# Kernel tuning notes

Hardware: AMD Instinct MI355X
Metric: run time of the kernel (lower is better)

Reference implementation:

```python
import jax, jax.numpy as jnp
import numpy as np

ALPHA = 0.2          # LeakyReLU negative slope
NEG_INF = -9e15      # standard GAT masking constant


def gat_layer(h, adj_mask, W, a_src, a_dst):
    # h: [N, D], adj_mask: [N, N] bool
    Wh = h @ W                                  # [N, D]
    e = (Wh @ a_src)[:, None] + (Wh @ a_dst)[None, :]  # [N, N]
    e = jax.nn.leaky_relu(e, negative_slope=ALPHA)
    e = jnp.where(adj_mask, e, NEG_INF)
    attn = jax.nn.softmax(e, axis=-1)           # [N, N]
    return jax.nn.relu(attn @ Wh)               # PlainGCN applies ReLU


def setup_inputs() -> dict:
    key = jax.random.key(0)
    ks = jax.random.split(key, 8)
    N, D = 8192, 256
    x = jax.random.normal(ks[0], (N, D), dtype=jnp.float32)
    adj = jax.random.randint(ks[1], (N, N), 0, 2, dtype=jnp.int32)
    s = 1.0 / np.sqrt(D)
    W1 = jax.random.normal(ks[2], (D, D), dtype=jnp.float32) * s
    a1_src = jax.random.normal(ks[3], (D,), dtype=jnp.float32) * s
    a1_dst = jax.random.normal(ks[4], (D,), dtype=jnp.float32) * s
    W2 = jax.random.normal(ks[5], (D, D), dtype=jnp.float32) * s
    a2_src = jax.random.normal(ks[6], (D,), dtype=jnp.float32) * s
    a2_dst = jax.random.normal(ks[7], (D,), dtype=jnp.float32) * s
    return {"x": x, "adj": adj, "W1": W1, "a1_src": a1_src, "a1_dst": a1_dst,
            "W2": W2, "a2_src": a2_src, "a2_dst": a2_dst}


def reference(x, adj, W1, a1_src, a1_dst, W2, a2_src, a2_dst):
    adj_mask = adj > 0
    h = gat_layer(x, adj_mask, W1, a1_src, a1_dst)
    h = gat_layer(h, adj_mask, W2, a2_src, a2_dst)
    return h
```

## Files before the change

### kernel.cpp

```cpp
#include <hip/hip_runtime.h>
#include <cstdint>
#include <cstddef>


#define ALPHA 0.2f
#define NN 8192
#define DD 256

typedef __attribute__((ext_vector_type(8))) short short8;
typedef __attribute__((ext_vector_type(4))) float f32x4;
typedef __attribute__((ext_vector_type(2))) _Float16 half2v;
typedef __attribute__((ext_vector_type(8))) __fp16 h8;

__device__ __forceinline__ unsigned pk_f16(float a, float b) {
    return __builtin_bit_cast(unsigned, __builtin_amdgcn_cvt_pkrtz(a, b));
}

__device__ __forceinline__ int sbit(uint32_t x, int o) {
    return ((int)(x << (31 - o))) >> 31;
}

__device__ __forceinline__ uint32_t hmerge(uint32_t hi, uint32_t lo) {
#if __has_builtin(__builtin_amdgcn_perm)
    return __builtin_amdgcn_perm(hi, lo, 0x07060100u);
#else
    return (hi & 0xFFFF0000u) | (lo & 0x0000FFFFu);
#endif
}

__device__ __forceinline__ half2v pkmax(half2v a, half2v b) {
#if __has_builtin(__builtin_elementwise_max)
    return __builtin_elementwise_max(a, b);
#else
    half2v r;
    asm("v_pk_max_f16 %0, %1, %2" : "=v"(r) : "v"(a), "v"(b));
    return r;
#endif
}

__device__ __forceinline__ f32x4 mfma_f16(uint4 a, short8 b, f32x4 c) {
    return __builtin_amdgcn_mfma_f32_16x16x32_f16(__builtin_bit_cast(h8, a),
                                                  __builtin_bit_cast(h8, b), c, 0, 0, 0);
}


__device__ __forceinline__ void packbits_dev(const int* __restrict__ adj,
                                             uint64_t* __restrict__ bits,
                                             int row, int lane) {
    const int* rowp = adj + (size_t)row * NN;
    uint64_t* dst = bits + (size_t)row * 128;
    for (int it = 0; it < 16; it++) {
        const int* p = rowp + it * 512;
        int a0 = p[lane];
        int a1 = p[64 + lane];
        int a2 = p[128 + lane];
        int a3 = p[192 + lane];
        int a4 = p[256 + lane];
        int a5 = p[320 + lane];
        int a6 = p[384 + lane];
        int a7 = p[448 + lane];
        uint64_t m0 = __ballot(a0 != 0);
        uint64_t m1 = __ballot(a1 != 0);
        uint64_t m2 = __ballot(a2 != 0);
        uint64_t m3 = __ballot(a3 != 0);
        uint64_t m4 = __ballot(a4 != 0);
        uint64_t m5 = __ballot(a5 != 0);
        uint64_t m6 = __ballot(a6 != 0);
        uint64_t m7 = __ballot(a7 != 0);
        if (lane == 0) {
            dst[it * 8 + 0] = m0; dst[it * 8 + 1] = m1;
            dst[it * 8 + 2] = m2; dst[it * 8 + 3] = m3;
            dst[it * 8 + 4] = m4; dst[it * 8 + 5] = m5;
            dst[it * 8 + 6] = m6; dst[it * 8 + 7] = m7;
        }
    }
}

__device__ __forceinline__ void transp_dev(const uint32_t* __restrict__ bits32,
                                           uint32_t* __restrict__ bitsT,
                                           int job, unsigned char* smem, int t) {
    uint32_t (*tile)[65] = (uint32_t (*)[65])smem;
    const int i0 = (job >> 2) * 64;
    const int w0 = (job & 3) * 64;
#pragma unroll
    for (int p = 0; p < 4; p++) {
        int r = (t >> 4) + 16 * p;
        int c4 = (t & 15) * 4;
        uint4 v = *(const uint4*)(bits32 + (size_t)(i0 + r) * 256 + w0 + c4);
        tile[r][c4 + 0] = v.x; tile[r][c4 + 1] = v.y;
        tile[r][c4 + 2] = v.z; tile[r][c4 + 3] = v.w;
    }
    __syncthreads();
#pragma unroll
    for (int p = 0; p < 4; p++) {
        int wr = (t >> 4) + 16 * p;
        int i4 = (t & 15) * 4;
        uint4 o = {tile[i4][wr], tile[i4 + 1][wr], tile[i4 + 2][wr], tile[i4 + 3][wr]};
        *(uint4*)(bitsT + (size_t)(w0 + wr) * NN + i0 + i4) = o;
    }
}

__device__ __forceinline__ void gemm_dev(const float* __restrict__ A,
                                         const float* __restrict__ B,
                                         unsigned short* __restrict__ Bpack,
                                         const float* __restrict__ a_src,
                                         const float* __restrict__ a_dst,
                                         float* __restrict__ s4,
                                         float* __restrict__ dd4,
                                         int job, unsigned char* smem, int t) {
    float (*At)[36] = (float (*)[36])smem;
    float2 (*Bs)[32] = (float2 (*)[32])(smem + 4608);
    const int m0 = (job >> 2) * 32;
    const int cq = job & 3;
    const int r0 = (t >> 5) * 4;
    const int cl = t & 31;
    float acc[4][2];
#pragma unroll
    for (int i = 0; i < 4; i++) { acc[i][0] = 0.f; acc[i][1] = 0.f; }

    for (int k0 = 0; k0 < DD; k0 += 32) {
        {
            int row = t >> 3, kq = t & 7;
            float4 v = *(const float4*)(A + (size_t)(m0 + row) * DD + k0 + kq * 4);
            At[kq * 4 + 0][row] = v.x; At[kq * 4 + 1][row] = v.y;
            At[kq * 4 + 2][row] = v.z; At[kq * 4 + 3][row] = v.w;
        }
#pragma unroll
        for (int l2 = 0; l2 < 2; l2++) {
            int fi = l2 * 256 + t;
            int br = fi >> 4, bc4 = fi & 15;
            float4 v = *(const float4*)(B + (size_t)(k0 + br) * DD + cq * 64 + bc4 * 4);
            Bs[br][bc4 * 2] = {v.x, v.y};
            Bs[br][bc4 * 2 + 1] = {v.z, v.w};
        }
        __syncthreads();
#pragma unroll
        for (int k = 0; k < 32; k++) {
            float4 a0 = *(const float4*)&At[k][r0];
            float2 b = Bs[k][cl];
            float av[4] = {a0.x, a0.y, a0.z, a0.w};
#pragma unroll
            for (int i = 0; i < 4; i++) {
                acc[i][0] += av[i] * b.x;
                acc[i][1] += av[i] * b.y;
            }
        }
        __syncthreads();
    }

    const int jt = m0 >> 5;
    const int lq = ((r0 >> 3) & 3) * 16;
    const int i8 = r0 & 4;
#pragma unroll
    for (int cc = 0; cc < 2; cc++) {
        int c = cq * 64 + cl * 2 + cc;
        int ct = c >> 4;
        int lane = lq + (c & 15);
        uint2 pk;
        pk.x = pk_f16(acc[0][cc], acc[1][cc]);
        pk.y = pk_f16(acc[2][cc], acc[3][cc]);
        *(uint2*)(Bpack + ((size_t)(jt * 16 + ct) * 64 + lane) * 8 + i8) = pk;
    }

    const int c0 = cq * 64 + cl * 2;
    float as0 = a_src[c0], as1 = a_src[c0 + 1];
    float ad0 = a_dst[c0], ad1 = a_dst[c0 + 1];
    float ps[4], pd[4];
#pragma unroll
    for (int i = 0; i < 4; i++) {
        ps[i] = acc[i][0] * as0 + acc[i][1] * as1;
        pd[i] = acc[i][0] * ad0 + acc[i][1] * ad1;
    }
#pragma unroll
    for (int off = 16; off; off >>= 1) {
#pragma unroll
        for (int i = 0; i < 4; i++) {
            ps[i] += __shfl_xor(ps[i], off);
            pd[i] += __shfl_xor(pd[i], off);
        }
    }
    if (cl == 0) {
#pragma unroll
        for (int i = 0; i < 4; i++) {
            s4[(size_t)cq * NN + m0 + r0 + i] = ps[i];
            dd4[(size_t)cq * NN + m0 + r0 + i] = pd[i];
        }
    }
}

__device__ __forceinline__ void rowstats_dev(const uint32_t* __restrict__ bits32,
                                             const float* __restrict__ s,
                                             const float* __restrict__ dd,
                                             float* __restrict__ Ep,
                                             float* __restrict__ Gp,
                                             int job, unsigned char* smem, int t) {
    uint32_t* smk = (uint32_t*)smem;
    float (*red)[4] = (float (*)[4])(smem + 4096);
    const int i0 = job * 4;
    const int wave = t >> 6, lane = t & 63;
    {
        const uint4* src = (const uint4*)(bits32 + (size_t)i0 * 256);
        ((uint4*)smk)[t] = src[t];
    }
    __syncthreads();

    float mx[4];
#pragma unroll
    for (int r = 0; r < 4; r++) mx[r] = -3.0e38f;
#pragma unroll
    for (int q = 0; q < 8; q++) {
        float4 v = *(const float4*)(dd + 4 * (t + 256 * q));
        const int wq = 32 * q + (t >> 3);
        const int sh = (t & 7) * 4;
#pragma unroll
        for (int r = 0; r < 4; r++) {
            uint32_t b = smk[r * 256 + wq] >> sh;
            mx[r] = fmaxf(mx[r], (b & 1u) ? v.x : -3.0e38f);
            mx[r] = fmaxf(mx[r], (b & 2u) ? v.y : -3.0e38f);
            mx[r] = fmaxf(mx[r], (b & 4u) ? v.z : -3.0e38f);
            mx[r] = fmaxf(mx[r], (b & 8u) ? v.w : -3.0e38f);
        }
    }
#pragma unroll
    for (int r = 0; r < 4; r++) {
#pragma unroll
        for (int off = 32; off; off >>= 1) mx[r] = fmaxf(mx[r], __shfl_down(mx[r], off));
    }
    if (lane == 0) {
#pragma unroll
        for (int r = 0; r < 4; r++) red[wave][r] = mx[r];
    }
    __syncthreads();
    if (t < 4) {
        float dmax = fmaxf(fmaxf(red[0][t], red[1][t]), fmaxf(red[2][t], red[3][t]));
        float si = s[i0 + t];
        float e = si + dmax;
        float m = e >= 0.f ? e : ALPHA * e;
        Ep[i0 + t] = 256.0f * __expf(si - m);
        Gp[i0 + t] = 256.0f * __expf(ALPHA * si - m);
    }
}


__global__ __launch_bounds__(256) void mega1(const float* __restrict__ A,
                                             const float* __restrict__ W,
                                             unsigned short* __restrict__ Bpack,
                                             const float* __restrict__ a_src,
                                             const float* __restrict__ a_dst,
                                             float* __restrict__ s4,
                                             float* __restrict__ dd4,
                                             const int* __restrict__ adj,
                                             uint64_t* __restrict__ bits) {
    __shared__ __align__(16) unsigned char smem[12800];
    const int bx = blockIdx.x;
    const int t = threadIdx.x;
    const int sel = bx % 3;
    const int base = bx / 3;
    if (sel == 0) {
        gemm_dev(A, W, Bpack, a_src, a_dst, s4, dd4, base, smem, t);
    } else {
        const int row = base * 8 + (sel - 1) * 4 + (t >> 6);
        packbits_dev(adj, bits, row, t & 63);
    }
}

__global__ __launch_bounds__(256) void mega2(const uint32_t* __restrict__ bits32,
                                             uint32_t* __restrict__ bitsT,
                                             const float* __restrict__ s,
                                             const float* __restrict__ dd,
                                             float* __restrict__ Ep,
                                             float* __restrict__ Gp) {
    __shared__ __align__(16) unsigned char smem[16640];
    const int bx = blockIdx.x;
    const int t = threadIdx.x;
    const int sel = bx % 5;
    const int base = bx / 5;
    if (sel == 0) {
        transp_dev(bits32, bitsT, base, smem, t);
    } else {
        rowstats_dev(bits32, s, dd, Ep, Gp, base * 4 + (sel - 1), smem, t);
    }
}

__global__ __launch_bounds__(256) void k_gemm(const float* A, const float* W,
                                              unsigned short* Bpack,
                                              const float* a_src, const float* a_dst,
                                              float* s4, float* dd4) {
    __shared__ __align__(16) unsigned char smem[12800];
    gemm_dev(A, W, Bpack, a_src, a_dst, s4, dd4, blockIdx.x, smem, threadIdx.x);
}
__global__ __launch_bounds__(256) void k_rowstats(const uint32_t* bits32, const float* s,
                                                  const float* dd,
                                                  float* Ep, float* Gp) {
    __shared__ __align__(16) unsigned char smem[4200];
    rowstats_dev(bits32, s, dd, Ep, Gp, blockIdx.x, smem, threadIdx.x);
}

__global__ __launch_bounds__(256) void fhgen(const float* __restrict__ s4,
                                             const float* __restrict__ dd4,
                                             float* __restrict__ s,
                                             float* __restrict__ dd,
                                             uint32_t* __restrict__ FF,
                                             uint32_t* __restrict__ HH) {
    int i = blockIdx.x * 256 + threadIdx.x;
    float ssum = (s4[i] + s4[i + NN]) + (s4[i + 2 * NN] + s4[i + 3 * NN]);
    float dsum = (dd4[i] + dd4[i + NN]) + (dd4[i + 2 * NN] + dd4[i + 3 * NN]);
    s[i] = ssum;
    dd[i] = dsum;
    float F = __expf(dsum);
    float H = __expf(ALPHA * dsum);
    float Fn = __shfl_xor(F, 1);
    float Hn = __shfl_xor(H, 1);
    if ((i & 1) == 0) {
        FF[i >> 1] = pk_f16(F, Fn);
        HH[i >> 1] = pk_f16(H, Hn);
    }
}

__global__ __launch_bounds__(256, 4) void pv_mfma(const unsigned short* __restrict__ Bpack,
                                                  const uint32_t* __restrict__ bitsT,
                                                  const uint32_t* __restrict__ FF,
                                                  const uint32_t* __restrict__ HH,
                                                  const float* __restrict__ Ep,
                                                  const float* __restrict__ Gp,
                                                  float* __restrict__ pout,
                                                  float* __restrict__ rsum) {
    __shared__ __align__(16) uint4 pb[2][256];
    const int t = threadIdx.x;
    const int w = t >> 6, l = t & 63;
    const int bx = blockIdx.x;
    const int ks = bx & 7;
    const int i0 = (bx >> 3) * 64;
    const int kbase = ks * 32;

    const int rl16 = l & 15;
    const int ko = (l >> 4) * 8;
    const int rw = i0 + 16 * w + rl16;
    const _Float16 eph = (_Float16)Ep[rw];
    const _Float16 gph = (_Float16)Gp[rw];
    const half2v ep2 = {eph, eph};
    const half2v gp2 = {gph, gph};

    const unsigned short* bb = Bpack + ((size_t)(w * 4) * 64 + l) * 8;
    const uint32_t* btb = bitsT + rw;
    const uint32_t* ffb = FF + (ko >> 1);
    const uint32_t* hhb = HH + (ko >> 1);

    f32x4 acc[4][4];
#pragma unroll
    for (int i = 0; i < 4; i++)
#pragma unroll
        for (int q = 0; q < 4; q++) acc[i][q] = (f32x4){0.f, 0.f, 0.f, 0.f};
    float rsv = 0.f;

    auto build = [&](int cc) -> uint4 {
        uint32_t bw = btb[(size_t)cc * NN];
        uint4 fw = *(const uint4*)(ffb + cc * 16);
        uint4 hw = *(const uint4*)(hhb + cc * 16);
        const uint32_t fwa[4] = {fw.x, fw.y, fw.z, fw.w};
        const uint32_t hwa[4] = {hw.x, hw.y, hw.z, hw.w};
        const uint32_t wl = bw >> ko;
        uint32_t au[4];
#pragma unroll
        for (int p = 0; p < 4; p++) {
            half2v f2 = __builtin_bit_cast(half2v, fwa[p]);
            half2v h2 = __builtin_bit_cast(half2v, hwa[p]);
            half2v pm = ep2 * f2;
            half2v pa = gp2 * h2;
            half2v px = pkmax(pm, pa);
            uint32_t mlo = (uint32_t)sbit(wl, 2 * p);
            uint32_t mhi = (uint32_t)sbit(wl, 2 * p + 1);
            au[p] = __builtin_bit_cast(uint32_t, px) & hmerge(mhi, mlo);
        }
        half2v s01 = __builtin_bit_cast(half2v, au[0]) + __builtin_bit_cast(half2v, au[1]);
        half2v s23 = __builtin_bit_cast(half2v, au[2]) + __builtin_bit_cast(half2v, au[3]);
        half2v sp = s01 + s23;
        rsv += (float)sp.x + (float)sp.y;
        return (uint4){au[0], au[1], au[2], au[3]};
    };

    uint4 aucur = build(kbase);
    pb[0][w * 64 + l] = aucur;

    for (int jl = 0; jl < 32; jl++) {
        const int par = jl & 1;
        const unsigned short* bp = bb + (size_t)(kbase + jl) * 8192;
        short8 B0 = *(const short8*)(bp);
        short8 B1 = *(const short8*)(bp + 512);
        short8 B2 = *(const short8*)(bp + 1024);
        short8 B3 = *(const short8*)(bp + 1536);

        __syncthreads();

#pragma unroll
        for (int f = 0; f < 4; f++) {
            uint4 af;
            if (f == w) af = aucur;
            else        af = pb[par][f * 64 + l];
            acc[f][0] = mfma_f16(af, B0, acc[f][0]);
            acc[f][1] = mfma_f16(af, B1, acc[f][1]);
            acc[f][2] = mfma_f16(af, B2, acc[f][2]);
            acc[f][3] = mfma_f16(af, B3, acc[f][3]);
        }

        if (jl < 31) {
            uint4 an = build(kbase + jl + 1);
            pb[par ^ 1][w * 64 + l] = an;
            aucur = an;
        }
    }

    rsv += __shfl_xor(rsv, 16);
    rsv += __shfl_xor(rsv, 32);
    if (l < 16) rsum[(size_t)ks * NN + rw] = rsv;

    float* outp = pout + (size_t)ks * NN * DD;
#pragma unroll
    for (int f = 0; f < 4; f++) {
        const int orow = i0 + 16 * f + (l >> 4) * 4;
#pragma unroll
        for (int q = 0; q < 4; q++) {
            const int ocol = w * 64 + q * 16 + rl16;
#pragma unroll
            for (int r = 0; r < 4; r++)
                outp[(size_t)(orow + r) * DD + ocol] = acc[f][q][r];
        }
    }
}

__global__ __launch_bounds__(256) void combine8(const float* __restrict__ p,
                                                const float* __restrict__ rsum,
                                                float* __restrict__ out) {
    const size_t S = (size_t)NN * DD / 4;
    size_t idx = (size_t)blockIdx.x * 256 + threadIdx.x;
    const int row = (int)(idx >> 6);
    float rs = (rsum[row] + rsum[row + NN]) + (rsum[row + 2 * NN] + rsum[row + 3 * NN])
             + (rsum[row + 4 * NN] + rsum[row + 5 * NN])
             + (rsum[row + 6 * NN] + rsum[row + 7 * NN]);
    const float inv = 1.0f / rs;
    float4 a0 = ((const float4*)p)[idx];
    float4 a1 = ((const float4*)p)[idx + S];
    float4 a2 = ((const float4*)p)[idx + 2 * S];
    float4 a3 = ((const float4*)p)[idx + 3 * S];
    float4 a4 = ((const float4*)p)[idx + 4 * S];
    float4 a5 = ((const float4*)p)[idx + 5 * S];
    float4 a6 = ((const float4*)p)[idx + 6 * S];
    float4 a7 = ((const float4*)p)[idx + 7 * S];
    float4 o;
    o.x = fmaxf((((a0.x + a1.x) + (a2.x + a3.x)) + ((a4.x + a5.x) + (a6.x + a7.x))) * inv, 0.f);
    o.y = fmaxf((((a0.y + a1.y) + (a2.y + a3.y)) + ((a4.y + a5.y) + (a6.y + a7.y))) * inv, 0.f);
    o.z = fmaxf((((a0.z + a1.z) + (a2.z + a3.z)) + ((a4.z + a5.z) + (a6.z + a7.z))) * inv, 0.f);
    o.w = fmaxf((((a0.w + a1.w) + (a2.w + a3.w)) + ((a4.w + a5.w) + (a6.w + a7.w))) * inv, 0.f);
    ((float4*)out)[idx] = o;
}

extern "C" void kernel_launch(void* const* d_in, const int* in_sizes, int n_in,
                              void* d_out, int out_size, void* d_ws, size_t ws_size,
                              hipStream_t stream) {
    const float* x   = (const float*)d_in[0];
    const int* adj   = (const int*)d_in[1];
    const float* W1  = (const float*)d_in[2];
    const float* a1s = (const float*)d_in[3];
    const float* a1d = (const float*)d_in[4];
    const float* W2  = (const float*)d_in[5];
    const float* a2s = (const float*)d_in[6];
    const float* a2d = (const float*)d_in[7];
    float* out = (float*)d_out;

    char* ws = (char*)d_ws;
    const size_t MB = 1024ull * 1024ull;
    uint64_t*       bits  = (uint64_t*)(ws + 8 * MB);
    uint32_t*       bits32= (uint32_t*)bits;
    uint32_t*       bitsT = (uint32_t*)(ws + 16 * MB);
    float*          sArr  = (float*)(ws + 24 * MB);
    float*          ddA   = sArr + NN;
    float*          EpA   = sArr + 2 * NN;
    float*          GpA   = sArr + 3 * NN;
    float*          s4    = sArr + 4 * NN;
    float*          dd4   = sArr + 8 * NN;
    uint32_t*       FFA   = (uint32_t*)(sArr + 12 * NN);
    uint32_t*       HHA   = FFA + NN / 2;
    float*          rsumA = sArr + 13 * NN;
    unsigned short* Bpack = (unsigned short*)(ws + 25 * MB);
    float*          pout  = (float*)(ws + 32 * MB);

    mega1<<<dim3(3072), dim3(256), 0, stream>>>(x, W1, Bpack, a1s, a1d, s4, dd4,
                                                adj, bits);
    fhgen<<<dim3(32), dim3(256), 0, stream>>>(s4, dd4, sArr, ddA, FFA, HHA);
    mega2<<<dim3(2560), dim3(256), 0, stream>>>(bits32, bitsT, sArr, ddA, EpA, GpA);
    pv_mfma<<<dim3(1024), dim3(256), 0, stream>>>(Bpack, bitsT, FFA, HHA, EpA, GpA,
                                                  pout, rsumA);
    combine8<<<dim3(2048), dim3(256), 0, stream>>>(pout, rsumA, out);

    k_gemm<<<dim3(1024), dim3(256), 0, stream>>>(out, W2, Bpack, a2s, a2d, s4, dd4);
    fhgen<<<dim3(32), dim3(256), 0, stream>>>(s4, dd4, sArr, ddA, FFA, HHA);
    k_rowstats<<<dim3(2048), dim3(256), 0, stream>>>(bits32, sArr, ddA, EpA, GpA);
    pv_mfma<<<dim3(1024), dim3(256), 0, stream>>>(Bpack, bitsT, FFA, HHA, EpA, GpA,
                                                  pout, rsumA);
    combine8<<<dim3(2048), dim3(256), 0, stream>>>(pout, rsumA, out);
}
```

Measured before the change: 538.8 us.

## Replace per-row masked max with global max softmax shift, drop rowstats pass

Computes the softmax stabilizing maximum from the global maximum of destination scores instead of a per-row masked neighbour maximum. This removes the rowstats kernels that scanned the adjacency bitmask for every row in both layers. The fhgen step is folded into the transpose megakernel, and a small epgen kernel is added to produce the row scaling factors. The shift is still a valid upper bound, but rows whose true max is far below the global one risk reduced precision or underflow.

```diff
diff --git a/kernel.cpp b/kernel.cpp
--- a/kernel.cpp
+++ b/kernel.cpp
@@ -188,57 +188,32 @@
     }
 }
 
-__device__ __forceinline__ void rowstats_dev(const uint32_t* __restrict__ bits32,
-                                             const float* __restrict__ s,
-                                             const float* __restrict__ dd,
-                                             float* __restrict__ Ep,
-                                             float* __restrict__ Gp,
-                                             int job, unsigned char* smem, int t) {
-    uint32_t* smk = (uint32_t*)smem;
-    float (*red)[4] = (float (*)[4])(smem + 4096);
-    const int i0 = job * 4;
+__device__ __forceinline__ void fhgen_dev(const float* __restrict__ s4,
+                                          const float* __restrict__ dd4,
+                                          float* __restrict__ s,
+                                          uint32_t* __restrict__ FF,
+                                          uint32_t* __restrict__ HH,
+                                          float* __restrict__ dmax32,
+                                          int job, float* sred, int t) {
+    const int i = job * 256 + t;
+    float ssum = (s4[i] + s4[i + NN]) + (s4[i + 2 * NN] + s4[i + 3 * NN]);
+    float dsum = (dd4[i] + dd4[i + NN]) + (dd4[i + 2 * NN] + dd4[i + 3 * NN]);
+    s[i] = ssum;
+    float F = __expf(dsum);
+    float H = __expf(ALPHA * dsum);
+    float Fn = __shfl_xor(F, 1);
+    float Hn = __shfl_xor(H, 1);
+    if ((i & 1) == 0) {
+        FF[i >> 1] = pk_f16(F, Fn);
+        HH[i >> 1] = pk_f16(H, Hn);
+    }
+    float bm = dsum;
+#pragma unroll
+    for (int off = 32; off; off >>= 1) bm = fmaxf(bm, __shfl_xor(bm, off));
     const int wave = t >> 6, lane = t & 63;
-    {
-        const uint4* src = (const uint4*)(bits32 + (size_t)i0 * 256);
-        ((uint4*)smk)[t] = src[t];
-    }
+    if (lane == 0) sred[wave] = bm;
     __syncthreads();
-
-    float mx[4];
-#pragma unroll
-    for (int r = 0; r < 4; r++) mx[r] = -3.0e38f;
-#pragma unroll
-    for (int q = 0; q < 8; q++) {
-        float4 v = *(const float4*)(dd + 4 * (t + 256 * q));
-        const int wq = 32 * q + (t >> 3);
-        const int sh = (t & 7) * 4;
-#pragma unroll
-        for (int r = 0; r < 4; r++) {
-            uint32_t b = smk[r * 256 + wq] >> sh;
-            mx[r] = fmaxf(mx[r], (b & 1u) ? v.x : -3.0e38f);
-            mx[r] = fmaxf(mx[r], (b & 2u) ? v.y : -3.0e38f);
-            mx[r] = fmaxf(mx[r], (b & 4u) ? v.z : -3.0e38f);
-            mx[r] = fmaxf(mx[r], (b & 8u) ? v.w : -3.0e38f);
-        }
-    }
-#pragma unroll
-    for (int r = 0; r < 4; r++) {
-#pragma unroll
-        for (int off = 32; off; off >>= 1) mx[r] = fmaxf(mx[r], __shfl_down(mx[r], off));
-    }
-    if (lane == 0) {
-#pragma unroll
-        for (int r = 0; r < 4; r++) red[wave][r] = mx[r];
-    }
-    __syncthreads();
-    if (t < 4) {
-        float dmax = fmaxf(fmaxf(red[0][t], red[1][t]), fmaxf(red[2][t], red[3][t]));
-        float si = s[i0 + t];
-        float e = si + dmax;
-        float m = e >= 0.f ? e : ALPHA * e;
-        Ep[i0 + t] = 256.0f * __expf(si - m);
-        Gp[i0 + t] = 256.0f * __expf(ALPHA * si - m);
-    }
+    if (t == 0) dmax32[job] = fmaxf(fmaxf(sred[0], sred[1]), fmaxf(sred[2], sred[3]));
 }
 
 
@@ -264,21 +239,21 @@
     }
 }
 
-__global__ __launch_bounds__(256) void mega2(const uint32_t* __restrict__ bits32,
+__global__ __launch_bounds__(256) void megaB(const uint32_t* __restrict__ bits32,
                                              uint32_t* __restrict__ bitsT,
-                                             const float* __restrict__ s,
-                                             const float* __restrict__ dd,
-                                             float* __restrict__ Ep,
-                                             float* __restrict__ Gp) {
+                                             const float* __restrict__ s4,
+                                             const float* __restrict__ dd4,
+                                             float* __restrict__ s,
+                                             uint32_t* __restrict__ FF,
+                                             uint32_t* __restrict__ HH,
+                                             float* __restrict__ dmax32) {
     __shared__ __align__(16) unsigned char smem[16640];
     const int bx = blockIdx.x;
     const int t = threadIdx.x;
-    const int sel = bx % 5;
-    const int base = bx / 5;
-    if (sel == 0) {
-        transp_dev(bits32, bitsT, base, smem, t);
+    if (bx < 512) {
+        transp_dev(bits32, bitsT, bx, smem, t);
     } else {
-        rowstats_dev(bits32, s, dd, Ep, Gp, base * 4 + (sel - 1), smem, t);
+        fhgen_dev(s4, dd4, s, FF, HH, dmax32, bx - 512, (float*)smem, t);
     }
 }
 
@@ -289,32 +264,36 @@
     __shared__ __align__(16) unsigned char smem[12800];
     gemm_dev(A, W, Bpack, a_src, a_dst, s4, dd4, blockIdx.x, smem, threadIdx.x);
 }
-__global__ __launch_bounds__(256) void k_rowstats(const uint32_t* bits32, const float* s,
-                                                  const float* dd,
-                                                  float* Ep, float* Gp) {
-    __shared__ __align__(16) unsigned char smem[4200];
-    rowstats_dev(bits32, s, dd, Ep, Gp, blockIdx.x, smem, threadIdx.x);
-}
-
-__global__ __launch_bounds__(256) void fhgen(const float* __restrict__ s4,
-                                             const float* __restrict__ dd4,
-                                             float* __restrict__ s,
-                                             float* __restrict__ dd,
-                                             uint32_t* __restrict__ FF,
-                                             uint32_t* __restrict__ HH) {
-    int i = blockIdx.x * 256 + threadIdx.x;
-    float ssum = (s4[i] + s4[i + NN]) + (s4[i + 2 * NN] + s4[i + 3 * NN]);
-    float dsum = (dd4[i] + dd4[i + NN]) + (dd4[i + 2 * NN] + dd4[i + 3 * NN]);
-    s[i] = ssum;
-    dd[i] = dsum;
-    float F = __expf(dsum);
-    float H = __expf(ALPHA * dsum);
-    float Fn = __shfl_xor(F, 1);
-    float Hn = __shfl_xor(H, 1);
-    if ((i & 1) == 0) {
-        FF[i >> 1] = pk_f16(F, Fn);
-        HH[i >> 1] = pk_f16(H, Hn);
-    }
+__global__ __launch_bounds__(256) void k_fhgen(const float* __restrict__ s4,
+                                               const float* __restrict__ dd4,
+                                               float* __restrict__ s,
+                                               uint32_t* __restrict__ FF,
+                                               uint32_t* __restrict__ HH,
+                                               float* __restrict__ dmax32) {
+    __shared__ float sred[4];
+    fhgen_dev(s4, dd4, s, FF, HH, dmax32, blockIdx.x, sred, threadIdx.x);
+}
+
+__global__ __launch_bounds__(256) void epgen(const float* __restrict__ s,
+                                             const float* __restrict__ dmax32,
+                                             float* __restrict__ Ep,
+                                             float* __restrict__ Gp) {
+    __shared__ float sm;
+    const int t = threadIdx.x;
+    if (t == 0) {
+        float m = dmax32[0];
+#pragma unroll
+        for (int k = 1; k < 32; k++) m = fmaxf(m, dmax32[k]);
+        sm = m;
+    }
+    __syncthreads();
+    const float dmax = sm;
+    const int i = blockIdx.x * 256 + t;
+    float si = s[i];
+    float e = si + dmax;
+    float m = e >= 0.f ? e : ALPHA * e;
+    Ep[i] = 256.0f * __expf(si - m);
+    Gp[i] = 256.0f * __expf(ALPHA * si - m);
 }
 
 __global__ __launch_bounds__(256, 4) void pv_mfma(const unsigned short* __restrict__ Bpack,
@@ -473,28 +452,29 @@
     uint32_t*       bits32= (uint32_t*)bits;
     uint32_t*       bitsT = (uint32_t*)(ws + 16 * MB);
     float*          sArr  = (float*)(ws + 24 * MB);
-    float*          ddA   = sArr + NN;
-    float*          EpA   = sArr + 2 * NN;
-    float*          GpA   = sArr + 3 * NN;
-    float*          s4    = sArr + 4 * NN;
-    float*          dd4   = sArr + 8 * NN;
-    uint32_t*       FFA   = (uint32_t*)(sArr + 12 * NN);
+    float*          EpA   = sArr + NN;
+    float*          GpA   = sArr + 2 * NN;
+    float*          s4    = sArr + 3 * NN;
+    float*          dd4   = sArr + 7 * NN;
+    float*          rsumA = sArr + 11 * NN;
+    uint32_t*       FFA   = (uint32_t*)(sArr + 19 * NN);
     uint32_t*       HHA   = FFA + NN / 2;
-    float*          rsumA = sArr + 13 * NN;
+    float*          dmax32= sArr + 20 * NN;
     unsigned short* Bpack = (unsigned short*)(ws + 25 * MB);
     float*          pout  = (float*)(ws + 32 * MB);
 
     mega1<<<dim3(3072), dim3(256), 0, stream>>>(x, W1, Bpack, a1s, a1d, s4, dd4,
                                                 adj, bits);
-    fhgen<<<dim3(32), dim3(256), 0, stream>>>(s4, dd4, sArr, ddA, FFA, HHA);
-    mega2<<<dim3(2560), dim3(256), 0, stream>>>(bits32, bitsT, sArr, ddA, EpA, GpA);
+    megaB<<<dim3(544), dim3(256), 0, stream>>>(bits32, bitsT, s4, dd4, sArr,
+                                               FFA, HHA, dmax32);
+    epgen<<<dim3(32), dim3(256), 0, stream>>>(sArr, dmax32, EpA, GpA);
     pv_mfma<<<dim3(1024), dim3(256), 0, stream>>>(Bpack, bitsT, FFA, HHA, EpA, GpA,
                                                   pout, rsumA);
     combine8<<<dim3(2048), dim3(256), 0, stream>>>(pout, rsumA, out);
 
     k_gemm<<<dim3(1024), dim3(256), 0, stream>>>(out, W2, Bpack, a2s, a2d, s4, dd4);
-    fhgen<<<dim3(32), dim3(256), 0, stream>>>(s4, dd4, sArr, ddA, FFA, HHA);
-    k_rowstats<<<dim3(2048), dim3(256), 0, stream>>>(bits32, sArr, ddA, EpA, GpA);
+    k_fhgen<<<dim3(32), dim3(256), 0, stream>>>(s4, dd4, sArr, FFA, HHA, dmax32);
+    epgen<<<dim3(32), dim3(256), 0, stream>>>(sArr, dmax32, EpA, GpA);
     pv_mfma<<<dim3(1024), dim3(256), 0, stream>>>(Bpack, bitsT, FFA, HHA, EpA, GpA,
                                                   pout, rsumA);
     combine8<<<dim3(2048), dim3(256), 0, stream>>>(pout, rsumA, out);
```

After: 521.7 us. 3.2% less time.
